# Kernel optimization log

Measured on AMD Instinct MI355X. Metric: run time of the kernel, lower is better.

The kernel has to match this reference:

```python
import jax, jax.numpy as jnp
import numpy as np

N, E, D, H, C, ED = 50000, 800000, 128, 4, 32, 1
EFF = H * C  # 128 == D, so residual proj is Identity
FFN_H = 2 * EFF


def setup_inputs() -> dict:
    key = jax.random.key(0)
    ks = jax.random.split(key, 16)
    def p(k, shape, fan_in):
        return jax.random.normal(k, shape, dtype=jnp.float32) / np.sqrt(fan_in)
    return {
        "x": jax.random.normal(ks[0], (N, D), dtype=jnp.float32),
        "edge_attr": jax.random.normal(ks[1], (E, ED), dtype=jnp.float32),
        "W_l": p(ks[2], (D, EFF), D),
        "b_l": jnp.zeros((EFF,), jnp.float32),
        "W_r": p(ks[3], (D, EFF), D),
        "b_r": jnp.zeros((EFF,), jnp.float32),
        "W_e": p(ks[4], (ED, EFF), ED),
        "att": p(ks[5], (H, C), C),
        "bias_out": jnp.zeros((EFF,), jnp.float32),
        "W_gate": p(ks[6], (EFF, 1), EFF),
        "b_gate": jnp.zeros((1,), jnp.float32),
        "W_ffn1": p(ks[7], (EFF, FFN_H), EFF),
        "b_ffn1": jnp.zeros((FFN_H,), jnp.float32),
        "W_ffn2": p(ks[8], (FFN_H, EFF), FFN_H),
        "b_ffn2": jnp.zeros((EFF,), jnp.float32),
        "ln_gamma": jnp.ones((EFF,), jnp.float32),
        "ln_beta": jnp.zeros((EFF,), jnp.float32),
        "edge_index": jax.random.randint(ks[9], (2, E), 0, N, dtype=jnp.int32),
    }


def _gat_block(x, edge_attr, W_l, b_l, W_r, b_r, W_e, att, bias_out,
               W_gate, b_gate, W_ffn1, b_ffn1, W_ffn2, b_ffn2,
               ln_gamma, ln_beta, edge_index):
    n = x.shape[0]
    # add self loops (PyG default), edge_attr filled with mean
    loop = jnp.arange(n, dtype=edge_index.dtype)
    src = jnp.concatenate([edge_index[0], loop])
    dst = jnp.concatenate([edge_index[1], loop])
    ea = jnp.concatenate([edge_attr,
                          jnp.broadcast_to(edge_attr.mean(0, keepdims=True), (n, edge_attr.shape[1]))])
    # GATv2: separate source/target transforms + edge embedding
    xl = (x @ W_l + b_l).reshape(n, H, C)   # source features
    xr = (x @ W_r + b_r).reshape(n, H, C)   # target features
    ee = (ea @ W_e).reshape(-1, H, C)
    xj = xl[src]                             # [Et,H,C]
    m = jax.nn.leaky_relu(xj + xr[dst] + ee, negative_slope=0.2)
    logits = jnp.einsum('ehc,hc->eh', m, att)           # [Et,H]
    # segment softmax over destination nodes
    mx = jax.ops.segment_max(logits, dst, num_segments=n)
    ex = jnp.exp(logits - mx[dst])
    den = jax.ops.segment_sum(ex, dst, num_segments=n)
    alpha = ex / den[dst]
    out = jax.ops.segment_sum(xj * alpha[..., None], dst, num_segments=n)
    out = out.reshape(n, EFF) + bias_out
    # block: ELU, gated residual (proj is Identity since D==EFF), FFN, LayerNorm
    h = jax.nn.elu(out)
    gate = jax.nn.sigmoid(h @ W_gate + b_gate)
    y = gate * h + (1.0 - gate) * x
    ffn = jax.nn.relu(y @ W_ffn1 + b_ffn1) @ W_ffn2 + b_ffn2
    y = y + ffn
    mu = y.mean(-1, keepdims=True)
    var = y.var(-1, keepdims=True)
    y = (y - mu) * jax.lax.rsqrt(var + 1e-5) * ln_gamma + ln_beta
    return y  # dropout is identity in eval mode


def reference(x, edge_attr, W_l, b_l, W_r, b_r, W_e, att, bias_out,
              W_gate, b_gate, W_ffn1, b_ffn1, W_ffn2, b_ffn2,
              ln_gamma, ln_beta, edge_index):
    return _gat_block(x, edge_attr, W_l, b_l, W_r, b_r, W_e, att, bias_out,
                      W_gate, b_gate, W_ffn1, b_ffn1, W_ffn2, b_ffn2,
                      ln_gamma, ln_beta, edge_index)
```

## Files before the change

kernel.cpp:

```cpp
#include <hip/hip_runtime.h>
#include <hip/hip_bf16.h>

#define NODES 50000
#define NEDGE 800000
#define ETOT  850000

#define NRANGE 49
#define SB 256
#define ES ((ETOT + SB - 1) / SB)

#define XF_TILES 1563
#define HIST_BLKS 256
#define FUSE_GRID (2 * HIST_BLKS + (XF_TILES - HIST_BLKS))

typedef __hip_bfloat16 bf16;
typedef __attribute__((ext_vector_type(8))) short bf16x8;
typedef __attribute__((ext_vector_type(4))) float f32x4;

__device__ __forceinline__ bf16 f2bf(float v) { return __float2bfloat16(v); }
__device__ __forceinline__ float bflo(unsigned int v) { return __uint_as_float(v << 16); }
__device__ __forceinline__ float bfhi(unsigned int v) { return __uint_as_float(v & 0xffff0000u); }

__device__ __forceinline__ unsigned int pack2(float a, float b) {
    bf16 x = f2bf(a), y = f2bf(b);
    unsigned short xs = *reinterpret_cast<unsigned short*>(&x);
    unsigned short ys = *reinterpret_cast<unsigned short*>(&y);
    return ((unsigned int)ys << 16) | (unsigned int)xs;
}

__device__ __forceinline__ unsigned short bfbits(float v) {
    bf16 x = f2bf(v);
    return *reinterpret_cast<unsigned short*>(&x);
}

__device__ __forceinline__ void split8(const float* v, bf16x8& hi, bf16x8& lo) {
    #pragma unroll
    for (int e = 0; e < 8; ++e) {
        unsigned short hb = bfbits(v[e]);
        float hv = __uint_as_float((unsigned int)hb << 16);
        unsigned short lb = bfbits(v[e] - hv);
        ((short*)&hi)[e] = (short)hb;
        ((short*)&lo)[e] = (short)lb;
    }
}

__global__ __launch_bounds__(256) void k_wxf(const float* W_l, const float* W_r,
                                             bf16* wlh, bf16* wll,
                                             bf16* wrh, bf16* wrl) {
    int tid = blockIdx.x * blockDim.x + threadIdx.x;
    int m = tid >> 14;
    int t = tid & 16383;
    int c = t >> 7, k = t & 127;
    const float* W = m ? W_r : W_l;
    float v = W[k * 128 + c];
    unsigned short hb = bfbits(v);
    float hv = __uint_as_float((unsigned int)hb << 16);
    bf16* dh = m ? wrh : wlh;
    bf16* dl = m ? wrl : wll;
    dh[t] = f2bf(v);
    dl[t] = f2bf(v - hv);
}

__global__ __launch_bounds__(256) void k_fuse(const float* edge_attr, const int* ei,
                                              float* sum_ea, int* rhist,
                                              const float* x,
                                              const bf16* wlh, const bf16* wll,
                                              const bf16* wrh, const bf16* wrl,
                                              const float* b_l, const float* b_r,
                                              bf16* xl, bf16* xr) {
    __shared__ __align__(16) float s_x[32][132];
    const int bid = blockIdx.x;
    int idx;
    bool isprep;
    if (bid < 2 * HIST_BLKS) { isprep = (bid & 1); idx = bid >> 1; }
    else { isprep = false; idx = HIST_BLKS + (bid - 2 * HIST_BLKS); }

    if (isprep) {
        int* hcnt = (int*)&s_x[0][0];
        const int t = threadIdx.x;
        if (t < 64) hcnt[t] = 0;
        __syncthreads();
        const int e0 = idx * ES;
        int e1 = e0 + ES; if (e1 > ETOT) e1 = ETOT;
        float local = 0.f;
        for (int e = e0 + t; e < e1; e += 256) {
            int dst = (e < NEDGE) ? ei[NEDGE + e] : (e - NEDGE);
            atomicAdd(&hcnt[dst >> 10], 1);
            if (e < NEDGE) local += edge_attr[e];
        }
        #pragma unroll
        for (int s = 1; s < 64; s <<= 1) local += __shfl_xor(local, s, 64);
        if ((t & 63) == 0) atomicAdd(sum_ea, local);
        __syncthreads();
        if (t < 64) rhist[idx * 64 + t] = hcnt[t];
        return;
    }

    const int tid = threadIdx.x;
    const int n0 = idx * 32;
    for (int it = 0; it < 4; ++it) {
        int idx4 = (it * 256 + tid) * 4;
        int n = idx4 >> 7, j = idx4 & 127;
        int node = n0 + n;
        float4 v = make_float4(0.f, 0.f, 0.f, 0.f);
        if (node < NODES) v = *(const float4*)(x + node * 128 + j);
        *(float4*)&s_x[n][j] = v;
    }
    __syncthreads();

    const int wv4  = tid >> 6;
    const int ln   = tid & 63;
    const int lrow = ln & 15;
    const int lk8  = (ln >> 4) << 3;
    const int m    = wv4 >> 1;
    const int cb   = (wv4 & 1) * 64;
    const bf16* Bh = m ? wrh : wlh;
    const bf16* Bl = m ? wrl : wll;
    const float* bias = m ? b_r : b_l;

    f32x4 acc[2][4];
    #pragma unroll
    for (int mt = 0; mt < 2; ++mt)
        #pragma unroll
        for (int i = 0; i < 4; ++i)
            acc[mt][i] = (f32x4){0.f, 0.f, 0.f, 0.f};
    #pragma unroll
    for (int kk = 0; kk < 4; ++kk) {
        int k0 = kk * 32 + lk8;
        float a0f[8], a1f[8];
        *(float4*)&a0f[0] = *(const float4*)&s_x[lrow][k0];
        *(float4*)&a0f[4] = *(const float4*)&s_x[lrow][k0 + 4];
        *(float4*)&a1f[0] = *(const float4*)&s_x[16 + lrow][k0];
        *(float4*)&a1f[4] = *(const float4*)&s_x[16 + lrow][k0 + 4];
        bf16x8 a0h, a0l, a1h, a1l;
        split8(a0f, a0h, a0l);
        split8(a1f, a1h, a1l);
        #pragma unroll
        for (int i = 0; i < 4; ++i) {
            int col = cb + (i << 4) + lrow;
            bf16x8 bh = *(const bf16x8*)(Bh + col * 128 + k0);
            bf16x8 bl = *(const bf16x8*)(Bl + col * 128 + k0);
            acc[0][i] = __builtin_amdgcn_mfma_f32_16x16x32_bf16(a0l, bh, acc[0][i], 0, 0, 0);
            acc[0][i] = __builtin_amdgcn_mfma_f32_16x16x32_bf16(a0h, bl, acc[0][i], 0, 0, 0);
            acc[0][i] = __builtin_amdgcn_mfma_f32_16x16x32_bf16(a0h, bh, acc[0][i], 0, 0, 0);
            acc[1][i] = __builtin_amdgcn_mfma_f32_16x16x32_bf16(a1l, bh, acc[1][i], 0, 0, 0);
            acc[1][i] = __builtin_amdgcn_mfma_f32_16x16x32_bf16(a1h, bl, acc[1][i], 0, 0, 0);
            acc[1][i] = __builtin_amdgcn_mfma_f32_16x16x32_bf16(a1h, bh, acc[1][i], 0, 0, 0);
        }
    }
    __syncthreads();
    bf16* s_o = (bf16*)&s_x[0][0];
    #pragma unroll
    for (int mt = 0; mt < 2; ++mt) {
        #pragma unroll
        for (int i = 0; i < 4; ++i) {
            int colg = cb + (i << 4) + lrow;
            float bv = bias[colg];
            #pragma unroll
            for (int r = 0; r < 4; ++r) {
                int row = (mt << 4) + ((ln >> 4) << 2) + r;
                s_o[row * 264 + m * 136 + colg] = f2bf(acc[mt][i][r] + bv);
            }
        }
    }
    __syncthreads();
    #pragma unroll
    for (int rep = 0; rep < 2; ++rep) {
        int idx2 = rep * 256 + tid;
        int row = idx2 >> 4, cc = (idx2 & 15) * 8;
        int node = n0 + row;
        if (node < NODES) {
            *(float4*)(xl + node * 128 + cc) = *(const float4*)(s_o + row * 264 + cc);
            *(float4*)(xr + node * 128 + cc) = *(const float4*)(s_o + row * 264 + 136 + cc);
        }
    }
}

__global__ __launch_bounds__(256) void k_rscan(int* rhist, int* base_r, int* off) {
    __shared__ int s_w[4];
    __shared__ int s_run;
    const int t = threadIdx.x, lane = t & 63, w = t >> 6;
    if (t == 0) s_run = 0;
    __syncthreads();
    for (int r = 0; r < NRANGE; ++r) {
        int v = rhist[t * 64 + r];
        int inc = v;
        #pragma unroll
        for (int d = 1; d < 64; d <<= 1) {
            int y = __shfl_up(inc, d, 64);
            if (lane >= d) inc += y;
        }
        if (lane == 63) s_w[w] = inc;
        __syncthreads();
        int woff = 0;
        #pragma unroll
        for (int ww = 0; ww < 4; ++ww) if (ww < w) woff += s_w[ww];
        int tot = s_w[0] + s_w[1] + s_w[2] + s_w[3];
        int runv = s_run;
        rhist[t * 64 + r] = runv + woff + (inc - v);
        if (t == 0) base_r[r] = runv;
        __syncthreads();
        if (t == 0) s_run = runv + tot;
        __syncthreads();
    }
    if (t == 0) { base_r[NRANGE] = ETOT; off[NODES] = ETOT; }
}

__global__ __launch_bounds__(256) void k_scatter(const int* ei, const float* edge_attr,
                                                 const float* sum_ea, const int* rhist,
                                                 uint2* tmp2) {
    __shared__ int cur[64];
    const int b = blockIdx.x, t = threadIdx.x;
    if (t < 64) cur[t] = rhist[b * 64 + t];
    __syncthreads();
    const float meanv = sum_ea[0] * (1.f / (float)NEDGE);
    const int e0 = b * ES;
    int e1 = e0 + ES; if (e1 > ETOT) e1 = ETOT;
    for (int e = e0 + t; e < e1; e += 256) {
        int src, dst; float eav;
        if (e < NEDGE) { src = ei[e]; dst = ei[NEDGE + e]; eav = edge_attr[e]; }
        else           { src = e - NEDGE; dst = src; eav = meanv; }
        int pos = atomicAdd(&cur[dst >> 10], 1);
        tmp2[pos] = make_uint2((unsigned int)dst,
                               ((unsigned int)bfbits(eav) << 16) | (unsigned int)src);
    }
}

__global__ __launch_bounds__(1024) void k_group(const uint2* tmp2, const int* base_r,
                                                int* off, unsigned int* perm) {
    __shared__ int lcnt[1024];
    __shared__ int s_w16[16];
    const int r = blockIdx.x, t = threadIdx.x;
    const int lane = t & 63, w = t >> 6;
    const int n0 = r << 10;
    const int s0 = base_r[r], s1 = base_r[r + 1];
    lcnt[t] = 0;
    __syncthreads();
    for (int i = s0 + t; i < s1; i += 1024) {
        int d = (int)tmp2[i].x;
        atomicAdd(&lcnt[d - n0], 1);
    }
    __syncthreads();
    int v = lcnt[t];
    int inc = v;
    #pragma unroll
    for (int d = 1; d < 64; d <<= 1) {
        int y = __shfl_up(inc, d, 64);
        if (lane >= d) inc += y;
    }
    if (lane == 63) s_w16[w] = inc;
    __syncthreads();
    int woff = 0;
    #pragma unroll
    for (int ww = 0; ww < 16; ++ww) if (ww < w) woff += s_w16[ww];
    int pos0 = s0 + woff + (inc - v);
    lcnt[t] = pos0;
    if (n0 + t < NODES) off[n0 + t] = pos0;
    __syncthreads();
    for (int i = s0 + t; i < s1; i += 1024) {
        uint2 p = tmp2[i];
        int pos = atomicAdd(&lcnt[(int)p.x - n0], 1);
        perm[pos] = p.y;
    }
}

__global__ __launch_bounds__(256) void k_wconv(const float* W1, const float* W2,
                                               bf16* w1h, bf16* w1l,
                                               bf16* w2h, bf16* w2l) {
    int tid = blockIdx.x * blockDim.x + threadIdx.x;
    if (tid < 32768) {
        int c = tid >> 7, k = tid & 127;
        float v = W1[k * 256 + c];
        unsigned short hb = bfbits(v);
        float hv = __uint_as_float((unsigned int)hb << 16);
        w1h[tid] = f2bf(v);
        w1l[tid] = f2bf(v - hv);
    } else {
        int t = tid - 32768;
        int c = t >> 8, k = t & 255;
        float v = W2[k * 128 + c];
        unsigned short hb = bfbits(v);
        float hv = __uint_as_float((unsigned int)hb << 16);
        w2h[t] = f2bf(v);
        w2l[t] = f2bf(v - hv);
    }
}

__global__ __launch_bounds__(256) void k_agg(const unsigned int* xl32,
                                             const unsigned int* xr32,
                                             const unsigned int* perm, const int* off,
                                             const float* W_e, const float* att,
                                             float* outp) {
    const int lane = threadIdx.x & 63;
    const int wave0 = blockIdx.x * 4 + (threadIdx.x >> 6);
    const int nwaves = gridDim.x * 4;
    const int c = 2 * lane;
    const float we1 = W_e[c], we2 = W_e[c + 1];
    const float a1 = att[c], a2 = att[c + 1];
    for (int n = wave0; n < NODES; n += nwaves) {
        unsigned int xru = xr32[n * 64 + lane];
        float xr1 = bflo(xru), xr2 = bfhi(xru);
        int s0 = off[n], s1 = off[n + 1];
        float m = -1e30f, l = 0.f, acc1 = 0.f, acc2 = 0.f;
        int j = s0;
        for (; j + 4 <= s1; j += 4) {
            unsigned int u0 = perm[j];
            unsigned int u1 = perm[j + 1];
            unsigned int u2 = perm[j + 2];
            unsigned int u3 = perm[j + 3];
            unsigned int g0 = xl32[(u0 & 0xffffu) * 64 + lane];
            unsigned int g1 = xl32[(u1 & 0xffffu) * 64 + lane];
            unsigned int g2 = xl32[(u2 & 0xffffu) * 64 + lane];
            unsigned int g3 = xl32[(u3 & 0xffffu) * 64 + lane];
            float e0 = bfhi(u0), e1 = bfhi(u1), e2 = bfhi(u2), e3 = bfhi(u3);
            float x01 = bflo(g0), x02 = bfhi(g0);
            float x11 = bflo(g1), x12 = bfhi(g1);
            float x21 = bflo(g2), x22 = bfhi(g2);
            float x31 = bflo(g3), x32 = bfhi(g3);
            float p0, p1, p2, p3;
            {
                float v1 = x01 + xr1 + e0 * we1, v2 = x02 + xr2 + e0 * we2;
                v1 = (v1 > 0.f) ? v1 : 0.2f * v1;
                v2 = (v2 > 0.f) ? v2 : 0.2f * v2;
                p0 = v1 * a1 + v2 * a2;
            }
            {
                float v1 = x11 + xr1 + e1 * we1, v2 = x12 + xr2 + e1 * we2;
                v1 = (v1 > 0.f) ? v1 : 0.2f * v1;
                v2 = (v2 > 0.f) ? v2 : 0.2f * v2;
                p1 = v1 * a1 + v2 * a2;
            }
            {
                float v1 = x21 + xr1 + e2 * we1, v2 = x22 + xr2 + e2 * we2;
                v1 = (v1 > 0.f) ? v1 : 0.2f * v1;
                v2 = (v2 > 0.f) ? v2 : 0.2f * v2;
                p2 = v1 * a1 + v2 * a2;
            }
            {
                float v1 = x31 + xr1 + e3 * we1, v2 = x32 + xr2 + e3 * we2;
                v1 = (v1 > 0.f) ? v1 : 0.2f * v1;
                v2 = (v2 > 0.f) ? v2 : 0.2f * v2;
                p3 = v1 * a1 + v2 * a2;
            }
            p0 += __shfl_xor(p0, 1, 64); p1 += __shfl_xor(p1, 1, 64);
            p2 += __shfl_xor(p2, 1, 64); p3 += __shfl_xor(p3, 1, 64);
            p0 += __shfl_xor(p0, 2, 64); p1 += __shfl_xor(p1, 2, 64);
            p2 += __shfl_xor(p2, 2, 64); p3 += __shfl_xor(p3, 2, 64);
            p0 += __shfl_xor(p0, 4, 64); p1 += __shfl_xor(p1, 4, 64);
            p2 += __shfl_xor(p2, 4, 64); p3 += __shfl_xor(p3, 4, 64);
            p0 += __shfl_xor(p0, 8, 64); p1 += __shfl_xor(p1, 8, 64);
            p2 += __shfl_xor(p2, 8, 64); p3 += __shfl_xor(p3, 8, 64);
            float nm = fmaxf(fmaxf(m, fmaxf(p0, p1)), fmaxf(p2, p3));
            float sc = __expf(m - nm);
            float E0 = __expf(p0 - nm);
            float E1 = __expf(p1 - nm);
            float E2 = __expf(p2 - nm);
            float E3 = __expf(p3 - nm);
            l = l * sc + E0 + E1 + E2 + E3;
            acc1 = acc1 * sc + E0 * x01 + E1 * x11 + E2 * x21 + E3 * x31;
            acc2 = acc2 * sc + E0 * x02 + E1 * x12 + E2 * x22 + E3 * x32;
            m = nm;
        }
        for (; j < s1; ++j) {
            unsigned int u0 = perm[j];
            unsigned int g0 = xl32[(u0 & 0xffffu) * 64 + lane];
            float e0 = bfhi(u0);
            float x01 = bflo(g0), x02 = bfhi(g0);
            float v1 = x01 + xr1 + e0 * we1, v2 = x02 + xr2 + e0 * we2;
            v1 = (v1 > 0.f) ? v1 : 0.2f * v1;
            v2 = (v2 > 0.f) ? v2 : 0.2f * v2;
            float p = v1 * a1 + v2 * a2;
            p += __shfl_xor(p, 1, 64);
            p += __shfl_xor(p, 2, 64);
            p += __shfl_xor(p, 4, 64);
            p += __shfl_xor(p, 8, 64);
            float nm = fmaxf(m, p);
            float sc = __expf(m - nm);
            float ee = __expf(p - nm);
            l = l * sc + ee;
            acc1 = acc1 * sc + ee * x01;
            acc2 = acc2 * sc + ee * x02;
            m = nm;
        }
        float inv = 1.f / fmaxf(l, 1e-30f);
        *(float2*)(outp + n * 128 + c) = make_float2(acc1 * inv, acc2 * inv);
    }
}

__global__ __launch_bounds__(256) void k_epi(const float* out_agg, const float* x,
                                             const float* bias_out,
                                             const float* W_gate, const float* b_gate,
                                             const bf16* w1h, const bf16* w1l,
                                             const float* b_ffn1,
                                             const bf16* w2h, const bf16* w2l,
                                             const float* b_ffn2,
                                             const float* gamma, const float* beta,
                                             float* out) {
    __shared__ __align__(16) float s_y[32][132];
    __shared__ __align__(16) float s_t[32][260];
    __shared__ float s_g[32];
    __shared__ float s_mu[32], s_rs[32];
    const int tid = threadIdx.x;
    const int n0 = blockIdx.x * 32;
    int nn = NODES - n0; if (nn > 32) nn = 32;

    for (int it = 0; it < 4; ++it) {
        int idx4 = (it * 256 + tid) * 4;
        int n = idx4 >> 7, j = idx4 & 127;
        float4 w = make_float4(0.f, 0.f, 0.f, 0.f);
        if (n < nn) {
            float4 v  = *(const float4*)(out_agg + (n0 + n) * 128 + j);
            float4 bv = *(const float4*)(bias_out + j);
            float t0 = v.x + bv.x, t1 = v.y + bv.y;
            float t2 = v.z + bv.z, t3 = v.w + bv.w;
            w.x = (t0 > 0.f) ? t0 : (__expf(t0) - 1.f);
            w.y = (t1 > 0.f) ? t1 : (__expf(t1) - 1.f);
            w.z = (t2 > 0.f) ? t2 : (__expf(t2) - 1.f);
            w.w = (t3 > 0.f) ? t3 : (__expf(t3) - 1.f);
        }
        *(float4*)&s_y[n][j] = w;
    }
    __syncthreads();
    {
        int n = tid >> 3, kb = (tid & 7) * 16;
        float g = 0.f;
        #pragma unroll
        for (int k = 0; k < 16; k += 4) {
            float4 w = *(const float4*)(W_gate + kb + k);
            float4 h = *(const float4*)&s_y[n][kb + k];
            g += h.x * w.x + h.y * w.y + h.z * w.z + h.w * w.w;
        }
        g += __shfl_xor(g, 1, 64);
        g += __shfl_xor(g, 2, 64);
        g += __shfl_xor(g, 4, 64);
        if ((tid & 7) == 0) s_g[n] = 1.f / (1.f + __expf(-(g + b_gate[0])));
    }
    __syncthreads();
    for (int it = 0; it < 4; ++it) {
        int idx4 = (it * 256 + tid) * 4;
        int n = idx4 >> 7, j = idx4 & 127;
        if (n < nn) {
            float g = s_g[n];
            float4 xv = *(const float4*)(x + (n0 + n) * 128 + j);
            float4 h = *(float4*)&s_y[n][j];
            h.x = g * h.x + (1.f - g) * xv.x;
            h.y = g * h.y + (1.f - g) * xv.y;
            h.z = g * h.z + (1.f - g) * xv.z;
            h.w = g * h.w + (1.f - g) * xv.w;
            *(float4*)&s_y[n][j] = h;
        }
    }
    __syncthreads();

    const int wv   = tid >> 6;
    const int ln   = tid & 63;
    const int lrow = ln & 15;
    const int lk8  = (ln >> 4) << 3;

    f32x4 acc1[2][4];
    #pragma unroll
    for (int mt = 0; mt < 2; ++mt)
        #pragma unroll
        for (int i = 0; i < 4; ++i)
            acc1[mt][i] = (f32x4){0.f, 0.f, 0.f, 0.f};
    #pragma unroll
    for (int kk = 0; kk < 4; ++kk) {
        int k0 = kk * 32 + lk8;
        float a0f[8], a1f[8];
        *(float4*)&a0f[0] = *(const float4*)&s_y[lrow][k0];
        *(float4*)&a0f[4] = *(const float4*)&s_y[lrow][k0 + 4];
        *(float4*)&a1f[0] = *(const float4*)&s_y[16 + lrow][k0];
        *(float4*)&a1f[4] = *(const float4*)&s_y[16 + lrow][k0 + 4];
        bf16x8 a0h, a0l, a1h, a1l;
        split8(a0f, a0h, a0l);
        split8(a1f, a1h, a1l);
        #pragma unroll
        for (int i = 0; i < 4; ++i) {
            int col = (wv << 6) + (i << 4) + lrow;
            bf16x8 bh = *(const bf16x8*)(w1h + col * 128 + k0);
            bf16x8 bl = *(const bf16x8*)(w1l + col * 128 + k0);
            acc1[0][i] = __builtin_amdgcn_mfma_f32_16x16x32_bf16(a0l, bh, acc1[0][i], 0, 0, 0);
            acc1[0][i] = __builtin_amdgcn_mfma_f32_16x16x32_bf16(a0h, bl, acc1[0][i], 0, 0, 0);
            acc1[0][i] = __builtin_amdgcn_mfma_f32_16x16x32_bf16(a0h, bh, acc1[0][i], 0, 0, 0);
            acc1[1][i] = __builtin_amdgcn_mfma_f32_16x16x32_bf16(a1l, bh, acc1[1][i], 0, 0, 0);
            acc1[1][i] = __builtin_amdgcn_mfma_f32_16x16x32_bf16(a1h, bl, acc1[1][i], 0, 0, 0);
            acc1[1][i] = __builtin_amdgcn_mfma_f32_16x16x32_bf16(a1h, bh, acc1[1][i], 0, 0, 0);
        }
    }
    #pragma unroll
    for (int mt = 0; mt < 2; ++mt) {
        #pragma unroll
        for (int i = 0; i < 4; ++i) {
            int col = (wv << 6) + (i << 4) + lrow;
            float bv = b_ffn1[col];
            #pragma unroll
            for (int r = 0; r < 4; ++r) {
                int row = (mt << 4) + ((ln >> 4) << 2) + r;
                s_t[row][col] = fmaxf(acc1[mt][i][r] + bv, 0.f);
            }
        }
    }
    __syncthreads();

    f32x4 acc2[2][2];
    #pragma unroll
    for (int mt = 0; mt < 2; ++mt)
        #pragma unroll
        for (int c = 0; c < 2; ++c)
            acc2[mt][c] = (f32x4){0.f, 0.f, 0.f, 0.f};
    #pragma unroll
    for (int kk = 0; kk < 8; ++kk) {
        int k0 = kk * 32 + lk8;
        float a0f[8], a1f[8];
        *(float4*)&a0f[0] = *(const float4*)&s_t[lrow][k0];
        *(float4*)&a0f[4] = *(const float4*)&s_t[lrow][k0 + 4];
        *(float4*)&a1f[0] = *(const float4*)&s_t[16 + lrow][k0];
        *(float4*)&a1f[4] = *(const float4*)&s_t[16 + lrow][k0 + 4];
        bf16x8 a0h, a0l, a1h, a1l;
        split8(a0f, a0h, a0l);
        split8(a1f, a1h, a1l);
        #pragma unroll
        for (int c = 0; c < 2; ++c) {
            int col = (wv << 5) + (c << 4) + lrow;
            bf16x8 bh = *(const bf16x8*)(w2h + col * 256 + k0);
            bf16x8 bl = *(const bf16x8*)(w2l + col * 256 + k0);
            acc2[0][c] = __builtin_amdgcn_mfma_f32_16x16x32_bf16(a0l, bh, acc2[0][c], 0, 0, 0);
            acc2[0][c] = __builtin_amdgcn_mfma_f32_16x16x32_bf16(a0h, bl, acc2[0][c], 0, 0, 0);
            acc2[0][c] = __builtin_amdgcn_mfma_f32_16x16x32_bf16(a0h, bh, acc2[0][c], 0, 0, 0);
            acc2[1][c] = __builtin_amdgcn_mfma_f32_16x16x32_bf16(a1l, bh, acc2[1][c], 0, 0, 0);
            acc2[1][c] = __builtin_amdgcn_mfma_f32_16x16x32_bf16(a1h, bl, acc2[1][c], 0, 0, 0);
            acc2[1][c] = __builtin_amdgcn_mfma_f32_16x16x32_bf16(a1h, bh, acc2[1][c], 0, 0, 0);
        }
    }
    #pragma unroll
    for (int mt = 0; mt < 2; ++mt) {
        #pragma unroll
        for (int c = 0; c < 2; ++c) {
            int col = (wv << 5) + (c << 4) + lrow;
            float bv = b_ffn2[col];
            #pragma unroll
            for (int r = 0; r < 4; ++r) {
                int row = (mt << 4) + ((ln >> 4) << 2) + r;
                s_y[row][col] += acc2[mt][c][r] + bv;
            }
        }
    }
    __syncthreads();
    {
        int n = tid >> 3, kb = (tid & 7) * 16;
        float s = 0.f, ss = 0.f;
        #pragma unroll
        for (int k = 0; k < 16; k += 4) {
            float4 v = *(const float4*)&s_y[n][kb + k];
            s  += v.x + v.y + v.z + v.w;
            ss += v.x * v.x + v.y * v.y + v.z * v.z + v.w * v.w;
        }
        s  += __shfl_xor(s, 1, 64);  ss += __shfl_xor(ss, 1, 64);
        s  += __shfl_xor(s, 2, 64);  ss += __shfl_xor(ss, 2, 64);
        s  += __shfl_xor(s, 4, 64);  ss += __shfl_xor(ss, 4, 64);
        if ((tid & 7) == 0) {
            float mu = s * (1.f / 128.f);
            float var = ss * (1.f / 128.f) - mu * mu;
            s_mu[n] = mu;
            s_rs[n] = rsqrtf(fmaxf(var, 0.f) + 1e-5f);
        }
    }
    __syncthreads();
    for (int it = 0; it < 4; ++it) {
        int idx4 = (it * 256 + tid) * 4;
        int n = idx4 >> 7, j = idx4 & 127;
        if (n < nn) {
            float mu = s_mu[n], rs = s_rs[n];
            float4 gv = *(const float4*)(gamma + j);
            float4 bv = *(const float4*)(beta + j);
            float4 v = *(const float4*)&s_y[n][j];
            float4 o;
            o.x = (v.x - mu) * rs * gv.x + bv.x;
            o.y = (v.y - mu) * rs * gv.y + bv.y;
            o.z = (v.z - mu) * rs * gv.z + bv.z;
            o.w = (v.w - mu) * rs * gv.w + bv.w;
            *(float4*)(out + (n0 + n) * 128 + j) = o;
        }
    }
}

extern "C" void kernel_launch(void* const* d_in, const int* in_sizes, int n_in,
                              void* d_out, int out_size, void* d_ws, size_t ws_size,
                              hipStream_t stream) {
    const float* x         = (const float*)d_in[0];
    const float* edge_attr = (const float*)d_in[1];
    const int* edge_index  = (const int*)d_in[17];
    float* out = (float*)d_out;

    char* base = (char*)d_ws;
    float* sum_ea  = (float*)(base + 16);
    int*   rhist   = (int*)  (base + 32);
    bf16*  w1t_hi  = (bf16*) (base + 32 + 65536);
    bf16*  w1t_lo  = (bf16*) (base + 32 + 131072);
    int*   off     = (int*)  (base + 200032);
    int*   base_r  = (int*)  (base + 400064);
    bf16*  w2t_hi  = (bf16*) (base + 400064 + 256);
    bf16*  w2t_lo  = (bf16*) (base + 400064 + 256 + 65536);
    unsigned int* perm = (unsigned int*)(base + 600064);
    bf16*  xl      = (bf16*) (base + 4000064);
    bf16*  xr      = (bf16*) (base + 16800064);
    bf16*  wxlh    = (bf16*) (base + 600064 + 1024);
    bf16*  wxll    = (bf16*) (base + 600064 + 1024 + 32768);
    bf16*  wxrh    = (bf16*) (base + 600064 + 1024 + 65536);
    bf16*  wxrl    = (bf16*) (base + 600064 + 1024 + 98304);
    uint2* tmp2    = (uint2*)d_out;

    hipMemsetAsync(sum_ea, 0, 16, stream);

    const int NTILES = (NODES + 31) / 32;

    k_wxf     <<<128, 256, 0, stream>>>((const float*)d_in[2], (const float*)d_in[4],
                                        wxlh, wxll, wxrh, wxrl);
    k_fuse    <<<FUSE_GRID, 256, 0, stream>>>(edge_attr, edge_index, sum_ea, rhist,
                                              x, wxlh, wxll, wxrh, wxrl,
                                              (const float*)d_in[3], (const float*)d_in[5],
                                              xl, xr);
    k_rscan   <<<1, 256, 0, stream>>>(rhist, base_r, off);
    k_scatter <<<SB, 256, 0, stream>>>(edge_index, edge_attr, sum_ea, rhist, tmp2);
    k_group   <<<NRANGE, 1024, 0, stream>>>(tmp2, base_r, off, perm);
    k_wconv   <<<256, 256, 0, stream>>>((const float*)d_in[11], (const float*)d_in[13],
                                        w1t_hi, w1t_lo, w2t_hi, w2t_lo);
    k_agg     <<<3125, 256, 0, stream>>>((const unsigned int*)xl,
                                         (const unsigned int*)xr,
                                         perm, off,
                                         (const float*)d_in[6], (const float*)d_in[7],
                                         out);
    k_epi     <<<NTILES, 256, 0, stream>>>(out, x, (const float*)d_in[8],
                                           (const float*)d_in[9], (const float*)d_in[10],
                                           w1t_hi, w1t_lo, (const float*)d_in[12],
                                           w2t_hi, w2t_lo, (const float*)d_in[14],
                                           (const float*)d_in[15], (const float*)d_in[16],
                                           out);
}
```

Baseline: 349.7 us.

## Fuse attention aggregation into epilogue kernel and merge weight conversion kernels

The per-node softmax aggregation now runs inside the epilogue kernel. Each of four waves in a block handles 8 of the block's 32 nodes and writes the ELU-activated result straight into shared memory. This removes the global write and re-read of the 50000x128 fp32 intermediate and one kernel launch. The two weight bf16 hi/lo conversion kernels are also merged into a single launch. In exchange, the gather phase now runs with only 1563 blocks and a fixed 8 nodes per wave instead of a grid-stride loop, so load balancing and latency hiding during the gather may suffer.

```diff
diff --git a/kernel.cpp b/kernel.cpp
--- a/kernel.cpp
+++ b/kernel.cpp
@@ -33,32 +33,49 @@
     return *reinterpret_cast<unsigned short*>(&x);
 }
 
+__device__ __forceinline__ void hilo(float v, unsigned short& h, unsigned short& l) {
+    h = bfbits(v);
+    float hv = __uint_as_float((unsigned int)h << 16);
+    l = bfbits(v - hv);
+}
+
 __device__ __forceinline__ void split8(const float* v, bf16x8& hi, bf16x8& lo) {
     #pragma unroll
     for (int e = 0; e < 8; ++e) {
-        unsigned short hb = bfbits(v[e]);
-        float hv = __uint_as_float((unsigned int)hb << 16);
-        unsigned short lb = bfbits(v[e] - hv);
+        unsigned short hb, lb;
+        hilo(v[e], hb, lb);
         ((short*)&hi)[e] = (short)hb;
         ((short*)&lo)[e] = (short)lb;
     }
 }
 
-__global__ __launch_bounds__(256) void k_wxf(const float* W_l, const float* W_r,
-                                             bf16* wlh, bf16* wll,
-                                             bf16* wrh, bf16* wrl) {
+__global__ __launch_bounds__(256) void k_wx(const float* W_l, const float* W_r,
+                                            const float* W1, const float* W2,
+                                            bf16* wlh, bf16* wll,
+                                            bf16* wrh, bf16* wrl,
+                                            bf16* w1h, bf16* w1l,
+                                            bf16* w2h, bf16* w2l) {
     int tid = blockIdx.x * blockDim.x + threadIdx.x;
-    int m = tid >> 14;
-    int t = tid & 16383;
-    int c = t >> 7, k = t & 127;
-    const float* W = m ? W_r : W_l;
-    float v = W[k * 128 + c];
-    unsigned short hb = bfbits(v);
-    float hv = __uint_as_float((unsigned int)hb << 16);
-    bf16* dh = m ? wrh : wlh;
-    bf16* dl = m ? wrl : wll;
-    dh[t] = f2bf(v);
-    dl[t] = f2bf(v - hv);
+    unsigned short h, l;
+    if (tid < 32768) {
+        int m = tid >> 14, t = tid & 16383;
+        int c = t >> 7, k = t & 127;
+        hilo((m ? W_r : W_l)[k * 128 + c], h, l);
+        (m ? wrh : wlh)[t] = *(bf16*)&h;
+        (m ? wrl : wll)[t] = *(bf16*)&l;
+    } else if (tid < 65536) {
+        int t = tid - 32768;
+        int c = t >> 7, k = t & 127;
+        hilo(W1[k * 256 + c], h, l);
+        w1h[t] = *(bf16*)&h;
+        w1l[t] = *(bf16*)&l;
+    } else {
+        int t = tid - 65536;
+        int c = t >> 8, k = t & 255;
+        hilo(W2[k * 128 + c], h, l);
+        w2h[t] = *(bf16*)&h;
+        w2l[t] = *(bf16*)&l;
+    }
 }
 
 __global__ __launch_bounds__(256) void k_fuse(const float* edge_attr, const int* ei,
@@ -264,161 +281,132 @@
     }
 }
 
-__global__ __launch_bounds__(256) void k_wconv(const float* W1, const float* W2,
-                                               bf16* w1h, bf16* w1l,
-                                               bf16* w2h, bf16* w2l) {
-    int tid = blockIdx.x * blockDim.x + threadIdx.x;
-    if (tid < 32768) {
-        int c = tid >> 7, k = tid & 127;
-        float v = W1[k * 256 + c];
-        unsigned short hb = bfbits(v);
-        float hv = __uint_as_float((unsigned int)hb << 16);
-        w1h[tid] = f2bf(v);
-        w1l[tid] = f2bf(v - hv);
-    } else {
-        int t = tid - 32768;
-        int c = t >> 8, k = t & 255;
-        float v = W2[k * 128 + c];
-        unsigned short hb = bfbits(v);
-        float hv = __uint_as_float((unsigned int)hb << 16);
-        w2h[t] = f2bf(v);
-        w2l[t] = f2bf(v - hv);
-    }
-}
-
-__global__ __launch_bounds__(256) void k_agg(const unsigned int* xl32,
-                                             const unsigned int* xr32,
-                                             const unsigned int* perm, const int* off,
-                                             const float* W_e, const float* att,
-                                             float* outp) {
-    const int lane = threadIdx.x & 63;
-    const int wave0 = blockIdx.x * 4 + (threadIdx.x >> 6);
-    const int nwaves = gridDim.x * 4;
-    const int c = 2 * lane;
-    const float we1 = W_e[c], we2 = W_e[c + 1];
-    const float a1 = att[c], a2 = att[c + 1];
-    for (int n = wave0; n < NODES; n += nwaves) {
-        unsigned int xru = xr32[n * 64 + lane];
-        float xr1 = bflo(xru), xr2 = bfhi(xru);
-        int s0 = off[n], s1 = off[n + 1];
-        float m = -1e30f, l = 0.f, acc1 = 0.f, acc2 = 0.f;
-        int j = s0;
-        for (; j + 4 <= s1; j += 4) {
-            unsigned int u0 = perm[j];
-            unsigned int u1 = perm[j + 1];
-            unsigned int u2 = perm[j + 2];
-            unsigned int u3 = perm[j + 3];
-            unsigned int g0 = xl32[(u0 & 0xffffu) * 64 + lane];
-            unsigned int g1 = xl32[(u1 & 0xffffu) * 64 + lane];
-            unsigned int g2 = xl32[(u2 & 0xffffu) * 64 + lane];
-            unsigned int g3 = xl32[(u3 & 0xffffu) * 64 + lane];
-            float e0 = bfhi(u0), e1 = bfhi(u1), e2 = bfhi(u2), e3 = bfhi(u3);
-            float x01 = bflo(g0), x02 = bfhi(g0);
-            float x11 = bflo(g1), x12 = bfhi(g1);
-            float x21 = bflo(g2), x22 = bfhi(g2);
-            float x31 = bflo(g3), x32 = bfhi(g3);
-            float p0, p1, p2, p3;
-            {
-                float v1 = x01 + xr1 + e0 * we1, v2 = x02 + xr2 + e0 * we2;
-                v1 = (v1 > 0.f) ? v1 : 0.2f * v1;
-                v2 = (v2 > 0.f) ? v2 : 0.2f * v2;
-                p0 = v1 * a1 + v2 * a2;
-            }
-            {
-                float v1 = x11 + xr1 + e1 * we1, v2 = x12 + xr2 + e1 * we2;
-                v1 = (v1 > 0.f) ? v1 : 0.2f * v1;
-                v2 = (v2 > 0.f) ? v2 : 0.2f * v2;
-                p1 = v1 * a1 + v2 * a2;
-            }
-            {
-                float v1 = x21 + xr1 + e2 * we1, v2 = x22 + xr2 + e2 * we2;
-                v1 = (v1 > 0.f) ? v1 : 0.2f * v1;
-                v2 = (v2 > 0.f) ? v2 : 0.2f * v2;
-                p2 = v1 * a1 + v2 * a2;
-            }
-            {
-                float v1 = x31 + xr1 + e3 * we1, v2 = x32 + xr2 + e3 * we2;
-                v1 = (v1 > 0.f) ? v1 : 0.2f * v1;
-                v2 = (v2 > 0.f) ? v2 : 0.2f * v2;
-                p3 = v1 * a1 + v2 * a2;
-            }
-            p0 += __shfl_xor(p0, 1, 64); p1 += __shfl_xor(p1, 1, 64);
-            p2 += __shfl_xor(p2, 1, 64); p3 += __shfl_xor(p3, 1, 64);
-            p0 += __shfl_xor(p0, 2, 64); p1 += __shfl_xor(p1, 2, 64);
-            p2 += __shfl_xor(p2, 2, 64); p3 += __shfl_xor(p3, 2, 64);
-            p0 += __shfl_xor(p0, 4, 64); p1 += __shfl_xor(p1, 4, 64);
-            p2 += __shfl_xor(p2, 4, 64); p3 += __shfl_xor(p3, 4, 64);
-            p0 += __shfl_xor(p0, 8, 64); p1 += __shfl_xor(p1, 8, 64);
-            p2 += __shfl_xor(p2, 8, 64); p3 += __shfl_xor(p3, 8, 64);
-            float nm = fmaxf(fmaxf(m, fmaxf(p0, p1)), fmaxf(p2, p3));
-            float sc = __expf(m - nm);
-            float E0 = __expf(p0 - nm);
-            float E1 = __expf(p1 - nm);
-            float E2 = __expf(p2 - nm);
-            float E3 = __expf(p3 - nm);
-            l = l * sc + E0 + E1 + E2 + E3;
-            acc1 = acc1 * sc + E0 * x01 + E1 * x11 + E2 * x21 + E3 * x31;
-            acc2 = acc2 * sc + E0 * x02 + E1 * x12 + E2 * x22 + E3 * x32;
-            m = nm;
-        }
-        for (; j < s1; ++j) {
-            unsigned int u0 = perm[j];
-            unsigned int g0 = xl32[(u0 & 0xffffu) * 64 + lane];
-            float e0 = bfhi(u0);
-            float x01 = bflo(g0), x02 = bfhi(g0);
-            float v1 = x01 + xr1 + e0 * we1, v2 = x02 + xr2 + e0 * we2;
-            v1 = (v1 > 0.f) ? v1 : 0.2f * v1;
-            v2 = (v2 > 0.f) ? v2 : 0.2f * v2;
-            float p = v1 * a1 + v2 * a2;
-            p += __shfl_xor(p, 1, 64);
-            p += __shfl_xor(p, 2, 64);
-            p += __shfl_xor(p, 4, 64);
-            p += __shfl_xor(p, 8, 64);
-            float nm = fmaxf(m, p);
-            float sc = __expf(m - nm);
-            float ee = __expf(p - nm);
-            l = l * sc + ee;
-            acc1 = acc1 * sc + ee * x01;
-            acc2 = acc2 * sc + ee * x02;
-            m = nm;
-        }
-        float inv = 1.f / fmaxf(l, 1e-30f);
-        *(float2*)(outp + n * 128 + c) = make_float2(acc1 * inv, acc2 * inv);
-    }
-}
-
-__global__ __launch_bounds__(256) void k_epi(const float* out_agg, const float* x,
-                                             const float* bias_out,
-                                             const float* W_gate, const float* b_gate,
-                                             const bf16* w1h, const bf16* w1l,
-                                             const float* b_ffn1,
-                                             const bf16* w2h, const bf16* w2l,
-                                             const float* b_ffn2,
-                                             const float* gamma, const float* beta,
-                                             float* out) {
+__global__ __launch_bounds__(256) void k_agge(const unsigned int* xl32,
+                                              const unsigned int* xr32,
+                                              const unsigned int* perm, const int* off,
+                                              const float* W_e, const float* att,
+                                              const float* bias_out,
+                                              const float* x,
+                                              const float* W_gate, const float* b_gate,
+                                              const bf16* w1h, const bf16* w1l,
+                                              const float* b_ffn1,
+                                              const bf16* w2h, const bf16* w2l,
+                                              const float* b_ffn2,
+                                              const float* gamma, const float* beta,
+                                              float* out) {
     __shared__ __align__(16) float s_y[32][132];
     __shared__ __align__(16) float s_t[32][260];
     __shared__ float s_g[32];
     __shared__ float s_mu[32], s_rs[32];
     const int tid = threadIdx.x;
+    const int lane = tid & 63;
+    const int wvi  = tid >> 6;
     const int n0 = blockIdx.x * 32;
     int nn = NODES - n0; if (nn > 32) nn = 32;
 
-    for (int it = 0; it < 4; ++it) {
-        int idx4 = (it * 256 + tid) * 4;
-        int n = idx4 >> 7, j = idx4 & 127;
-        float4 w = make_float4(0.f, 0.f, 0.f, 0.f);
-        if (n < nn) {
-            float4 v  = *(const float4*)(out_agg + (n0 + n) * 128 + j);
-            float4 bv = *(const float4*)(bias_out + j);
-            float t0 = v.x + bv.x, t1 = v.y + bv.y;
-            float t2 = v.z + bv.z, t3 = v.w + bv.w;
-            w.x = (t0 > 0.f) ? t0 : (__expf(t0) - 1.f);
-            w.y = (t1 > 0.f) ? t1 : (__expf(t1) - 1.f);
-            w.z = (t2 > 0.f) ? t2 : (__expf(t2) - 1.f);
-            w.w = (t3 > 0.f) ? t3 : (__expf(t3) - 1.f);
-        }
-        *(float4*)&s_y[n][j] = w;
+    {
+        const int c = 2 * lane;
+        const float we1 = W_e[c], we2 = W_e[c + 1];
+        const float a1 = att[c], a2 = att[c + 1];
+        const float bo1 = bias_out[c], bo2 = bias_out[c + 1];
+        for (int s = 0; s < 8; ++s) {
+            const int nl = wvi * 8 + s;
+            const int n = n0 + nl;
+            if (n < NODES) {
+                unsigned int xru = xr32[n * 64 + lane];
+                float xr1 = bflo(xru), xr2 = bfhi(xru);
+                int s0 = off[n], s1 = off[n + 1];
+                float m = -1e30f, l = 0.f, acc1 = 0.f, acc2 = 0.f;
+                int j = s0;
+                for (; j + 4 <= s1; j += 4) {
+                    unsigned int u0 = perm[j];
+                    unsigned int u1 = perm[j + 1];
+                    unsigned int u2 = perm[j + 2];
+                    unsigned int u3 = perm[j + 3];
+                    unsigned int g0 = xl32[(u0 & 0xffffu) * 64 + lane];
+                    unsigned int g1 = xl32[(u1 & 0xffffu) * 64 + lane];
+                    unsigned int g2 = xl32[(u2 & 0xffffu) * 64 + lane];
+                    unsigned int g3 = xl32[(u3 & 0xffffu) * 64 + lane];
+                    float e0 = bfhi(u0), e1 = bfhi(u1), e2 = bfhi(u2), e3 = bfhi(u3);
+                    float x01 = bflo(g0), x02 = bfhi(g0);
+                    float x11 = bflo(g1), x12 = bfhi(g1);
+                    float x21 = bflo(g2), x22 = bfhi(g2);
+                    float x31 = bflo(g3), x32 = bfhi(g3);
+                    float p0, p1, p2, p3;
+                    {
+                        float v1 = x01 + xr1 + e0 * we1, v2 = x02 + xr2 + e0 * we2;
+                        v1 = (v1 > 0.f) ? v1 : 0.2f * v1;
+                        v2 = (v2 > 0.f) ? v2 : 0.2f * v2;
+                        p0 = v1 * a1 + v2 * a2;
+                    }
+                    {
+                        float v1 = x11 + xr1 + e1 * we1, v2 = x12 + xr2 + e1 * we2;
+                        v1 = (v1 > 0.f) ? v1 : 0.2f * v1;
+                        v2 = (v2 > 0.f) ? v2 : 0.2f * v2;
+                        p1 = v1 * a1 + v2 * a2;
+                    }
+                    {
+                        float v1 = x21 + xr1 + e2 * we1, v2 = x22 + xr2 + e2 * we2;
+                        v1 = (v1 > 0.f) ? v1 : 0.2f * v1;
+                        v2 = (v2 > 0.f) ? v2 : 0.2f * v2;
+                        p2 = v1 * a1 + v2 * a2;
+                    }
+                    {
+                        float v1 = x31 + xr1 + e3 * we1, v2 = x32 + xr2 + e3 * we2;
+                        v1 = (v1 > 0.f) ? v1 : 0.2f * v1;
+                        v2 = (v2 > 0.f) ? v2 : 0.2f * v2;
+                        p3 = v1 * a1 + v2 * a2;
+                    }
+                    p0 += __shfl_xor(p0, 1, 64); p1 += __shfl_xor(p1, 1, 64);
+                    p2 += __shfl_xor(p2, 1, 64); p3 += __shfl_xor(p3, 1, 64);
+                    p0 += __shfl_xor(p0, 2, 64); p1 += __shfl_xor(p1, 2, 64);
+                    p2 += __shfl_xor(p2, 2, 64); p3 += __shfl_xor(p3, 2, 64);
+                    p0 += __shfl_xor(p0, 4, 64); p1 += __shfl_xor(p1, 4, 64);
+                    p2 += __shfl_xor(p2, 4, 64); p3 += __shfl_xor(p3, 4, 64);
+                    p0 += __shfl_xor(p0, 8, 64); p1 += __shfl_xor(p1, 8, 64);
+                    p2 += __shfl_xor(p2, 8, 64); p3 += __shfl_xor(p3, 8, 64);
+                    float nm = fmaxf(fmaxf(m, fmaxf(p0, p1)), fmaxf(p2, p3));
+                    float sc = __expf(m - nm);
+                    float E0 = __expf(p0 - nm);
+                    float E1 = __expf(p1 - nm);
+                    float E2 = __expf(p2 - nm);
+                    float E3 = __expf(p3 - nm);
+                    l = l * sc + E0 + E1 + E2 + E3;
+                    acc1 = acc1 * sc + E0 * x01 + E1 * x11 + E2 * x21 + E3 * x31;
+                    acc2 = acc2 * sc + E0 * x02 + E1 * x12 + E2 * x22 + E3 * x32;
+                    m = nm;
+                }
+                for (; j < s1; ++j) {
+                    unsigned int u0 = perm[j];
+                    unsigned int g0 = xl32[(u0 & 0xffffu) * 64 + lane];
+                    float e0 = bfhi(u0);
+                    float x01 = bflo(g0), x02 = bfhi(g0);
+                    float v1 = x01 + xr1 + e0 * we1, v2 = x02 + xr2 + e0 * we2;
+                    v1 = (v1 > 0.f) ? v1 : 0.2f * v1;
+                    v2 = (v2 > 0.f) ? v2 : 0.2f * v2;
+                    float p = v1 * a1 + v2 * a2;
+                    p += __shfl_xor(p, 1, 64);
+                    p += __shfl_xor(p, 2, 64);
+                    p += __shfl_xor(p, 4, 64);
+                    p += __shfl_xor(p, 8, 64);
+                    float nm = fmaxf(m, p);
+                    float sc = __expf(m - nm);
+                    float ee = __expf(p - nm);
+                    l = l * sc + ee;
+                    acc1 = acc1 * sc + ee * x01;
+                    acc2 = acc2 * sc + ee * x02;
+                    m = nm;
+                }
+                float inv = 1.f / fmaxf(l, 1e-30f);
+                float r1 = acc1 * inv + bo1;
+                float r2 = acc2 * inv + bo2;
+                r1 = (r1 > 0.f) ? r1 : (__expf(r1) - 1.f);
+                r2 = (r2 > 0.f) ? r2 : (__expf(r2) - 1.f);
+                *(float2*)&s_y[nl][c] = make_float2(r1, r2);
+            } else {
+                *(float2*)&s_y[nl][c] = make_float2(0.f, 0.f);
+            }
+        }
     }
     __syncthreads();
     {
@@ -452,8 +440,8 @@
     }
     __syncthreads();
 
-    const int wv   = tid >> 6;
-    const int ln   = tid & 63;
+    const int wv   = wvi;
+    const int ln   = lane;
     const int lrow = ln & 15;
     const int lk8  = (ln >> 4) << 3;
 
@@ -614,8 +602,10 @@
 
     const int NTILES = (NODES + 31) / 32;
 
-    k_wxf     <<<128, 256, 0, stream>>>((const float*)d_in[2], (const float*)d_in[4],
-                                        wxlh, wxll, wxrh, wxrl);
+    k_wx      <<<384, 256, 0, stream>>>((const float*)d_in[2], (const float*)d_in[4],
+                                        (const float*)d_in[11], (const float*)d_in[13],
+                                        wxlh, wxll, wxrh, wxrl,
+                                        w1t_hi, w1t_lo, w2t_hi, w2t_lo);
     k_fuse    <<<FUSE_GRID, 256, 0, stream>>>(edge_attr, edge_index, sum_ea, rhist,
                                               x, wxlh, wxll, wxrh, wxrl,
                                               (const float*)d_in[3], (const float*)d_in[5],
@@ -623,14 +613,11 @@
     k_rscan   <<<1, 256, 0, stream>>>(rhist, base_r, off);
     k_scatter <<<SB, 256, 0, stream>>>(edge_index, edge_attr, sum_ea, rhist, tmp2);
     k_group   <<<NRANGE, 1024, 0, stream>>>(tmp2, base_r, off, perm);
-    k_wconv   <<<256, 256, 0, stream>>>((const float*)d_in[11], (const float*)d_in[13],
-                                        w1t_hi, w1t_lo, w2t_hi, w2t_lo);
-    k_agg     <<<3125, 256, 0, stream>>>((const unsigned int*)xl,
-                                         (const unsigned int*)xr,
-                                         perm, off,
-                                         (const float*)d_in[6], (const float*)d_in[7],
-                                         out);
-    k_epi     <<<NTILES, 256, 0, stream>>>(out, x, (const float*)d_in[8],
+    k_agge    <<<NTILES, 256, 0, stream>>>((const unsigned int*)xl,
+                                           (const unsigned int*)xr,
+                                           perm, off,
+                                           (const float*)d_in[6], (const float*)d_in[7],
+                                           (const float*)d_in[8], x,
                                            (const float*)d_in[9], (const float*)d_in[10],
                                            w1t_hi, w1t_lo, (const float*)d_in[12],
                                            w2t_hi, w2t_lo, (const float*)d_in[14],
```

Result: slower. 391.3 us (+11.9%).
